# Optimization experiments

Hardware: AMD Instinct MI355X
Metric: run time of the kernel (lower is better)

The kernel has to match this reference:

```python
import jax, jax.numpy as jnp
import numpy as np

N = 80000        # nodes
E = 1280000      # edges
NG = 8           # graphs (segment ids)
F_IN = 3
NC = 20
BN_EPS = 1e-3    # keras BatchNormalization default epsilon


def setup_inputs() -> dict:
    key = jax.random.key(0)
    ks = jax.random.split(key, 16)
    inp = {}
    inp['x'] = jax.random.normal(ks[0], (N, F_IN), dtype=jnp.float32)
    inp['edge_w'] = jax.random.uniform(ks[1], (E,), dtype=jnp.float32)
    inp['src'] = jax.random.randint(ks[2], (E,), 0, N, dtype=jnp.int32)
    inp['dst'] = jax.random.randint(ks[3], (E,), 0, N, dtype=jnp.int32)
    inp['ids'] = jnp.sort(jax.random.randint(ks[4], (N,), 0, NG, dtype=jnp.int32))
    def w(k, fi, fo):
        return jax.random.normal(k, (fi, fo), dtype=jnp.float32) * (1.0 / np.sqrt(fi))
    inp['W1'] = w(ks[5], F_IN, 32); inp['b1'] = jnp.zeros((32,), jnp.float32)
    inp['W2'] = w(ks[6], 32, 32);   inp['b2'] = jnp.zeros((32,), jnp.float32)
    inp['g1'] = jnp.ones((32,), jnp.float32); inp['be1'] = jnp.zeros((32,), jnp.float32)
    inp['m1'] = jax.random.normal(ks[7], (32,), dtype=jnp.float32) * 0.1
    inp['v1'] = jax.random.uniform(ks[8], (32,), dtype=jnp.float32) + 0.5
    inp['W3'] = w(ks[9], 32, 64);   inp['b3'] = jnp.zeros((64,), jnp.float32)
    inp['W4'] = w(ks[10], 64, 64);  inp['b4'] = jnp.zeros((64,), jnp.float32)
    inp['g2'] = jnp.ones((64,), jnp.float32); inp['be2'] = jnp.zeros((64,), jnp.float32)
    inp['m2'] = jax.random.normal(ks[11], (64,), dtype=jnp.float32) * 0.1
    inp['v2'] = jax.random.uniform(ks[12], (64,), dtype=jnp.float32) + 0.5
    inp['W5'] = w(ks[13], 64, NC);  inp['b5'] = jnp.zeros((NC,), jnp.float32)
    return inp


def _gcn(x, W, b, src, dst, ew):
    # Spektral GCNConv: A_norm @ (X W) + b, with A given as edge list (src->dst).
    h = x @ W                                      # [N, Fo] dense transform first (cheaper)
    msg = h[src] * ew[:, None]                     # gather + scale  [E, Fo]
    agg = jax.ops.segment_sum(msg, dst, num_segments=N)  # scatter-add [N, Fo]
    return agg + b


def _bn(x, g, be, m, v):
    # inference-mode BatchNormalization
    return (x - m) * (g * jax.lax.rsqrt(v + BN_EPS)) + be


def _pool(x, ids):
    # per-graph global max pooling, broadcast back to nodes
    mx = jax.ops.segment_max(x, ids, num_segments=NG)   # [NG, F]
    return mx[ids]                                       # [N, F]


def reference(x, edge_w, src, dst, ids,
              W1, b1, W2, b2, g1, be1, m1, v1,
              W3, b3, W4, b4, g2, be2, m2, v2,
              W5, b5):
    h = jax.nn.relu(_gcn(x, W1, b1, src, dst, edge_w))
    h = jax.nn.relu(_gcn(h, W2, b2, src, dst, edge_w))
    h = _bn(h, g1, be1, m1, v1)
    h = _pool(h, ids)
    h = jax.nn.relu(_gcn(h, W3, b3, src, dst, edge_w))
    h = jax.nn.relu(_gcn(h, W4, b4, src, dst, edge_w))
    h = _bn(h, g2, be2, m2, v2)
    h = _pool(h, ids)
    # dropout is identity in inference
    out = jax.nn.softmax(_gcn(h, W5, b5, src, dst, edge_w), axis=-1)
    return out
```

## Files before the change

kernel.cpp:

```cpp
#include <hip/hip_runtime.h>

#define NN 80000
#define NE 1280000
#define NGR 8
#define BN_EPS 1e-3f
#define NBF 625
#define GB 1280
#define CHK 1000

typedef unsigned short ushort;
typedef __attribute__((ext_vector_type(8))) short bf16x8;
typedef __attribute__((ext_vector_type(4))) float f32x4;

__device__ __forceinline__ unsigned enc_f(float f) {
    unsigned b = __float_as_uint(f);
    return (f >= 0.f) ? (b | 0x80000000u) : ~b;
}
__device__ __forceinline__ float dec_f(unsigned u) {
    return (u & 0x80000000u) ? __uint_as_float(u & 0x7FFFFFFFu) : __uint_as_float(~u);
}
__device__ __forceinline__ ushort f2bf(float f) {
    unsigned u = __float_as_uint(f);
    unsigned r = u + 0x7FFFu + ((u >> 16) & 1u);
    return (ushort)(r >> 16);
}
__device__ __forceinline__ void fma8(float* acc, const ushort* p, float w) {
    uint4 q = *(const uint4*)p;
    acc[0] += w * __uint_as_float((q.x & 0xFFFFu) << 16);
    acc[1] += w * __uint_as_float(q.x & 0xFFFF0000u);
    acc[2] += w * __uint_as_float((q.y & 0xFFFFu) << 16);
    acc[3] += w * __uint_as_float(q.y & 0xFFFF0000u);
    acc[4] += w * __uint_as_float((q.z & 0xFFFFu) << 16);
    acc[5] += w * __uint_as_float(q.z & 0xFFFF0000u);
    acc[6] += w * __uint_as_float((q.w & 0xFFFFu) << 16);
    acc[7] += w * __uint_as_float(q.w & 0xFFFF0000u);
}

__global__ __launch_bounds__(256) void k_bhist(const int* __restrict__ dst,
                                               int* __restrict__ hcnt) {
    __shared__ int lh[NBF];
    for (int i = threadIdx.x; i < NBF; i += 256) lh[i] = 0;
    __syncthreads();
    int e0 = blockIdx.x * CHK;
    for (int e = e0 + threadIdx.x; e < e0 + CHK; e += 256)
        atomicAdd(&lh[dst[e] >> 7], 1);
    __syncthreads();
    int* row = hcnt + (size_t)blockIdx.x * NBF;
    for (int i = threadIdx.x; i < NBF; i += 256) row[i] = lh[i];
}

__global__ __launch_bounds__(256) void k_bbase1(int* __restrict__ hcnt,
                                                int* __restrict__ tot) {
    __shared__ int sm[256];
    int bin = blockIdx.x, t = threadIdx.x;
    int v[5];
    int s = 0;
    #pragma unroll
    for (int j = 0; j < 5; ++j) {
        v[j] = hcnt[(size_t)(t * 5 + j) * NBF + bin];
        s += v[j];
    }
    sm[t] = s;
    __syncthreads();
    #pragma unroll
    for (int off = 1; off < 256; off <<= 1) {
        int u = (t >= off) ? sm[t - off] : 0;
        __syncthreads();
        sm[t] += u;
        __syncthreads();
    }
    int run = sm[t] - s;
    if (t == 255) tot[bin] = sm[255];
    #pragma unroll
    for (int j = 0; j < 5; ++j) {
        hcnt[(size_t)(t * 5 + j) * NBF + bin] = run;
        run += v[j];
    }
}

__global__ __launch_bounds__(1024) void k_bbase2w(const int* __restrict__ tot,
                                                  int* __restrict__ bo,
                                                  const float* __restrict__ W2,
                                                  const float* __restrict__ W4,
                                                  ushort* __restrict__ W2t,
                                                  ushort* __restrict__ W4t) {
    __shared__ int sm[1024];
    int t = threadIdx.x;
    int v = (t < NBF) ? tot[t] : 0;
    sm[t] = v;
    __syncthreads();
    #pragma unroll
    for (int off = 1; off < 1024; off <<= 1) {
        int u = (t >= off) ? sm[t - off] : 0;
        __syncthreads();
        sm[t] += u;
        __syncthreads();
    }
    if (t < NBF) bo[t] = sm[t] - v;
    if (t == 0) bo[NBF] = NE;
    {
        int f = t >> 5, k = t & 31;
        W2t[t] = f2bf(W2[k * 32 + f]);
    }
    #pragma unroll
    for (int j = 0; j < 4; ++j) {
        int i = t + j * 1024;
        int f = i >> 6, k = i & 63;
        W4t[i] = f2bf(W4[k * 64 + f]);
    }
}

__global__ __launch_bounds__(256) void k_bfill(const int* __restrict__ src,
                                               const int* __restrict__ dst,
                                               const float* __restrict__ ew,
                                               const int* __restrict__ ids,
                                               const int* __restrict__ hcnt,
                                               const int* __restrict__ bo,
                                               int2* __restrict__ cB) {
    __shared__ int lcur[NBF];
    const int* row = hcnt + (size_t)blockIdx.x * NBF;
    for (int i = threadIdx.x; i < NBF; i += 256) lcur[i] = row[i] + bo[i];
    __syncthreads();
    int e0 = blockIdx.x * CHK;
    for (int e = e0 + threadIdx.x; e < e0 + CHK; e += 256) {
        int d = dst[e];
        int s = src[e];
        int pos = atomicAdd(&lcur[d >> 7], 1);
        cB[pos] = make_int2(s | (ids[s] << 17) | ((d & 127) << 20),
                            __float_as_int(ew[e]));
    }
}

__global__ __launch_bounds__(512) void k_insort(const int* __restrict__ bo,
                                                const int2* __restrict__ cB,
                                                const float* __restrict__ x,
                                                int* __restrict__ rp,
                                                int2* __restrict__ cE,
                                                float* __restrict__ S,
                                                float* __restrict__ AX) {
    __shared__ int lc[128];
    __shared__ int loff[128];
    __shared__ int sm[512];
    int bin = blockIdx.x, t = threadIdx.x;
    int s0 = bo[bin], s1 = bo[bin + 1];
    if (t < 128) lc[t] = 0;
    __syncthreads();
    for (int i = s0 + t; i < s1; i += 512)
        atomicAdd(&lc[(cB[i].x >> 20) & 127], 1);
    __syncthreads();
    int v = (t < 128) ? lc[t] : 0;
    sm[t] = v;
    __syncthreads();
    #pragma unroll
    for (int off = 1; off < 128; off <<= 1) {
        int u = (t >= off && t < 128) ? sm[t - off] : 0;
        __syncthreads();
        if (t < 128) sm[t] += u;
        __syncthreads();
    }
    if (t < 128) {
        loff[t] = sm[t] - v;
        rp[bin * 128 + t] = s0 + loff[t];
        lc[t] = 0;
    }
    if (bin == NBF - 1 && t == 0) rp[NN] = NE;
    __syncthreads();
    for (int i = s0 + t; i < s1; i += 512) {
        int2 a = cB[i];
        int dlow = (a.x >> 20) & 127;
        int pos = s0 + loff[dlow] + atomicAdd(&lc[dlow], 1);
        cE[pos] = make_int2((a.x & 0x1FFFF) | (((a.x >> 17) & 7) << 24), a.y);
    }
    __syncthreads();
    int n = t >> 2, q = t & 3;
    int ne0 = s0 + loff[n];
    int ne1 = ne0 + lc[n];
    float sv[8] = {0, 0, 0, 0, 0, 0, 0, 0};
    float ax0 = 0.f, ax1 = 0.f, ax2 = 0.f;
    for (int i = ne0 + q; i < ne1; i += 4) {
        int2 a = cE[i];
        float w = __int_as_float(a.y);
        int s = a.x & 0xFFFFFF;
        int gg = a.x >> 24;
        #pragma unroll
        for (int g = 0; g < 8; ++g) sv[g] += (gg == g) ? w : 0.f;
        const float* xp = x + s * 3;
        ax0 += w * xp[0]; ax1 += w * xp[1]; ax2 += w * xp[2];
    }
    #pragma unroll
    for (int g = 0; g < 8; ++g) {
        sv[g] += __shfl_xor(sv[g], 1);
        sv[g] += __shfl_xor(sv[g], 2);
    }
    ax0 += __shfl_xor(ax0, 1); ax0 += __shfl_xor(ax0, 2);
    ax1 += __shfl_xor(ax1, 1); ax1 += __shfl_xor(ax1, 2);
    ax2 += __shfl_xor(ax2, 1); ax2 += __shfl_xor(ax2, 2);
    if (q == 0) {
        int node = bin * 128 + n;
        float4* Sp = (float4*)(S + (size_t)node * 8);
        Sp[0] = make_float4(sv[0], sv[1], sv[2], sv[3]);
        Sp[1] = make_float4(sv[4], sv[5], sv[6], sv[7]);
        *(float4*)(AX + (size_t)node * 4) = make_float4(ax0, ax1, ax2, 0.f);
    }
}

__global__ __launch_bounds__(256) void k_l12m(const float* __restrict__ AX,
                                              const float* __restrict__ W1,
                                              const float* __restrict__ b1,
                                              const ushort* __restrict__ W2t,
                                              ushort* __restrict__ T) {
    __shared__ ushort h1s[64 * 40];
    int t = threadIdx.x;
    int nb = blockIdx.x * 64;
    {
        int f = t & 31, rr = t >> 5;
        float w0 = W1[f], w1 = W1[32 + f], w2 = W1[64 + f], bb = b1[f];
        #pragma unroll
        for (int i = 0; i < 8; ++i) {
            int n = rr + i * 8;
            float4 ax = *(const float4*)(AX + (nb + n) * 4);
            float acc = bb + ax.x * w0 + ax.y * w1 + ax.z * w2;
            h1s[n * 40 + f] = f2bf(fmaxf(acc, 0.f));
        }
    }
    __syncthreads();
    int lane = t & 63, wave = t >> 6;
    int quad = lane >> 4, col = lane & 15;
    int mtile = wave;
    bf16x8 a = *(const bf16x8*)(h1s + (mtile * 16 + col) * 40 + quad * 8);
    #pragma unroll
    for (int ntile = 0; ntile < 2; ++ntile) {
        bf16x8 b = *(const bf16x8*)(W2t + (ntile * 16 + col) * 32 + quad * 8);
        f32x4 acc = {0.f, 0.f, 0.f, 0.f};
        acc = __builtin_amdgcn_mfma_f32_16x16x32_bf16(a, b, acc, 0, 0, 0);
        #pragma unroll
        for (int r = 0; r < 4; ++r) {
            int node = nb + mtile * 16 + quad * 4 + r;
            T[node * 32 + ntile * 16 + col] = f2bf(acc[r]);
        }
    }
}

__global__ __launch_bounds__(256) void k_l34m(const float* __restrict__ S,
                                              const unsigned* __restrict__ mxe,
                                              const float* __restrict__ W3,
                                              const float* __restrict__ b3,
                                              const ushort* __restrict__ W4t,
                                              ushort* __restrict__ T) {
    __shared__ float smxs[256];
    __shared__ float HW3s[512];
    __shared__ ushort h3s[64 * 72];
    int t = threadIdx.x;
    int nb = blockIdx.x * 64;
    smxs[t] = mxe[t] ? dec_f(mxe[t]) : 0.f;
    __syncthreads();
    {
        #pragma unroll
        for (int j = 0; j < 2; ++j) {
            int i = t + j * 256;
            int g = i >> 6, f = i & 63;
            float acc = 0.f;
            #pragma unroll
            for (int k = 0; k < 32; ++k) acc += smxs[g * 32 + k] * W3[k * 64 + f];
            HW3s[i] = acc;
        }
    }
    __syncthreads();
    {
        int f = t & 63, rr = t >> 6;
        float hwc[8];
        #pragma unroll
        for (int g = 0; g < 8; ++g) hwc[g] = HW3s[g * 64 + f];
        float bb = b3[f];
        #pragma unroll
        for (int i = 0; i < 16; ++i) {
            int n = rr + i * 4;
            const float4* sp = (const float4*)(S + (size_t)(nb + n) * 8);
            float4 s0 = sp[0], s1 = sp[1];
            float acc = bb + s0.x * hwc[0] + s0.y * hwc[1] + s0.z * hwc[2] +
                        s0.w * hwc[3] + s1.x * hwc[4] + s1.y * hwc[5] +
                        s1.z * hwc[6] + s1.w * hwc[7];
            h3s[n * 72 + f] = f2bf(fmaxf(acc, 0.f));
        }
    }
    __syncthreads();
    int lane = t & 63, wave = t >> 6;
    int quad = lane >> 4, col = lane & 15;
    int mtile = wave;
    bf16x8 a0 = *(const bf16x8*)(h3s + (mtile * 16 + col) * 72 + quad * 8);
    bf16x8 a1 = *(const bf16x8*)(h3s + (mtile * 16 + col) * 72 + 32 + quad * 8);
    #pragma unroll
    for (int ntile = 0; ntile < 4; ++ntile) {
        bf16x8 b0 = *(const bf16x8*)(W4t + (ntile * 16 + col) * 64 + quad * 8);
        bf16x8 b1v = *(const bf16x8*)(W4t + (ntile * 16 + col) * 64 + 32 + quad * 8);
        f32x4 acc = {0.f, 0.f, 0.f, 0.f};
        acc = __builtin_amdgcn_mfma_f32_16x16x32_bf16(a0, b0, acc, 0, 0, 0);
        acc = __builtin_amdgcn_mfma_f32_16x16x32_bf16(a1, b1v, acc, 0, 0, 0);
        #pragma unroll
        for (int r = 0; r < 4; ++r) {
            int node = nb + mtile * 16 + quad * 4 + r;
            T[node * 64 + ntile * 16 + col] = f2bf(acc[r]);
        }
    }
}

template <int LOGF>
__global__ __launch_bounds__(256) void k_gpool(const ushort* __restrict__ th,
                                               const int* __restrict__ rp,
                                               const int2* __restrict__ cE,
                                               const int* __restrict__ ids,
                                               const float* __restrict__ b,
                                               const float* __restrict__ g,
                                               const float* __restrict__ be,
                                               const float* __restrict__ m,
                                               const float* __restrict__ v,
                                               unsigned* __restrict__ mxe) {
    const int F = 1 << LOGF;
    const int CPN = F >> 3;
    const int NPB = 256 / CPN;
    __shared__ unsigned lmx[NGR * F];
    for (int i = threadIdx.x; i < NGR * F; i += 256) lmx[i] = 0u;
    __syncthreads();
    int c = threadIdx.x & (CPN - 1);
    int n = blockIdx.x * NPB + (threadIdx.x >> (LOGF - 3));
    if (n < NN) {
        int e0 = rp[n], e1 = rp[n + 1];
        float a0[8] = {0, 0, 0, 0, 0, 0, 0, 0};
        float a1[8] = {0, 0, 0, 0, 0, 0, 0, 0};
        float a2[8] = {0, 0, 0, 0, 0, 0, 0, 0};
        float a3[8] = {0, 0, 0, 0, 0, 0, 0, 0};
        int i = e0;
        for (; i + 4 <= e1; i += 4) {
            int2 q0 = cE[i], q1 = cE[i + 1], q2 = cE[i + 2], q3 = cE[i + 3];
            fma8(a0, th + (((size_t)(q0.x & 0xFFFFFF)) << LOGF) + (c << 3), __int_as_float(q0.y));
            fma8(a1, th + (((size_t)(q1.x & 0xFFFFFF)) << LOGF) + (c << 3), __int_as_float(q1.y));
            fma8(a2, th + (((size_t)(q2.x & 0xFFFFFF)) << LOGF) + (c << 3), __int_as_float(q2.y));
            fma8(a3, th + (((size_t)(q3.x & 0xFFFFFF)) << LOGF) + (c << 3), __int_as_float(q3.y));
        }
        for (; i < e1; ++i) {
            int2 q0 = cE[i];
            fma8(a0, th + (((size_t)(q0.x & 0xFFFFFF)) << LOGF) + (c << 3), __int_as_float(q0.y));
        }
        int gg = ids[n];
        #pragma unroll
        for (int j = 0; j < 8; ++j) {
            int f = (c << 3) + j;
            float scale = g[f] * rsqrtf(v[f] + BN_EPS);
            float h = fmaxf((a0[j] + a1[j]) + (a2[j] + a3[j]) + b[f], 0.f);
            float val = (h - m[f]) * scale + be[f];
            atomicMax(&lmx[gg * F + f], enc_f(val));
        }
    }
    __syncthreads();
    for (int i = threadIdx.x; i < NGR * F; i += 256) {
        unsigned u = lmx[i];
        if (u) atomicMax(&mxe[i], u);
    }
}

__global__ __launch_bounds__(256) void k_out(const float* __restrict__ S,
                                             const unsigned* __restrict__ mxe,
                                             const float* __restrict__ W5,
                                             const float* __restrict__ b5,
                                             float* __restrict__ out) {
    __shared__ float smxs[512];
    __shared__ float hw[160];
    __shared__ float bb[20];
    int t = threadIdx.x;
    smxs[t] = mxe[t] ? dec_f(mxe[t]) : 0.f;
    smxs[t + 256] = mxe[t + 256] ? dec_f(mxe[t + 256]) : 0.f;
    if (t < 20) bb[t] = b5[t];
    __syncthreads();
    if (t < 160) {
        int g = t / 20, c = t % 20;
        float acc = 0.f;
        #pragma unroll
        for (int k = 0; k < 64; ++k) acc += smxs[g * 64 + k] * W5[k * 20 + c];
        hw[t] = acc;
    }
    __syncthreads();
    int n = blockIdx.x * 256 + t;
    if (n >= NN) return;
    const float4* sp = (const float4*)(S + (size_t)n * 8);
    float4 s0 = sp[0], s1 = sp[1];
    float sv[8] = {s0.x, s0.y, s0.z, s0.w, s1.x, s1.y, s1.z, s1.w};
    float pre[20];
    #pragma unroll
    for (int c = 0; c < 20; ++c) {
        float acc = bb[c];
        #pragma unroll
        for (int g = 0; g < 8; ++g) acc += sv[g] * hw[g * 20 + c];
        pre[c] = acc;
    }
    float mx = pre[0];
    #pragma unroll
    for (int c = 1; c < 20; ++c) mx = fmaxf(mx, pre[c]);
    float sum = 0.f;
    #pragma unroll
    for (int c = 0; c < 20; ++c) { pre[c] = __expf(pre[c] - mx); sum += pre[c]; }
    float inv = 1.f / sum;
    #pragma unroll
    for (int c = 0; c < 20; ++c) out[n * 20 + c] = pre[c] * inv;
}

extern "C" void kernel_launch(void* const* d_in, const int* in_sizes, int n_in,
                              void* d_out, int out_size, void* d_ws, size_t ws_size,
                              hipStream_t stream) {
    const float* x   = (const float*)d_in[0];
    const float* ew  = (const float*)d_in[1];
    const int*   src = (const int*)d_in[2];
    const int*   dst = (const int*)d_in[3];
    const int*   ids = (const int*)d_in[4];
    const float* W1 = (const float*)d_in[5];  const float* b1 = (const float*)d_in[6];
    const float* W2 = (const float*)d_in[7];  const float* b2 = (const float*)d_in[8];
    const float* g1 = (const float*)d_in[9];  const float* be1 = (const float*)d_in[10];
    const float* m1 = (const float*)d_in[11]; const float* v1 = (const float*)d_in[12];
    const float* W3 = (const float*)d_in[13]; const float* b3 = (const float*)d_in[14];
    const float* W4 = (const float*)d_in[15]; const float* b4 = (const float*)d_in[16];
    const float* g2 = (const float*)d_in[17]; const float* be2 = (const float*)d_in[18];
    const float* m2 = (const float*)d_in[19]; const float* v2 = (const float*)d_in[20];
    const float* W5 = (const float*)d_in[21]; const float* b5 = (const float*)d_in[22];
    float* out = (float*)d_out;

    char* p = (char*)d_ws;
    float*  S    = (float*)p;  p += (size_t)NN * 8 * 4;
    ushort* T    = (ushort*)p; p += (size_t)NN * 64 * 2;
    float*  AX   = (float*)p;  p += (size_t)NN * 4 * 4;
    int*    rp   = (int*)p;    p += (size_t)(NN + 16) * 4;
    int*    hcnt = (int*)p;    p += (size_t)GB * NBF * 4;
    int*    tot  = (int*)p;    p += 1024 * 4;
    int*    bo   = (int*)p;    p += 1024 * 4;
    int2*   cB   = (int2*)p;   p += (size_t)NE * 8;
    int2*   cE   = (int2*)p;   p += (size_t)NE * 8;
    unsigned* MXE1 = (unsigned*)p; p += 256 * 4;
    unsigned* MXE2 = (unsigned*)p; p += 512 * 4;
    ushort* W2t  = (ushort*)p; p += 1024 * 2;
    ushort* W4t  = (ushort*)p; p += 4096 * 2;

    const int BS = 256;
    const int gN = (NN + BS - 1) / BS;

    hipMemsetAsync(MXE1, 0, 768 * 4, stream);
    hipLaunchKernelGGL(k_bhist, dim3(GB), dim3(BS), 0, stream, dst, hcnt);
    hipLaunchKernelGGL(k_bbase1, dim3(NBF), dim3(BS), 0, stream, hcnt, tot);
    hipLaunchKernelGGL(k_bbase2w, dim3(1), dim3(1024), 0, stream, tot, bo, W2, W4, W2t, W4t);
    hipLaunchKernelGGL(k_bfill, dim3(GB), dim3(BS), 0, stream, src, dst, ew, ids, hcnt, bo, cB);
    hipLaunchKernelGGL(k_insort, dim3(NBF), dim3(512), 0, stream, bo, cB, x, rp, cE, S, AX);

    hipLaunchKernelGGL(k_l12m, dim3(NN / 64), dim3(BS), 0, stream, AX, W1, b1, W2t, T);
    hipLaunchKernelGGL(k_gpool<5>, dim3(NN / 64), dim3(BS), 0, stream, T, rp, cE, ids, b2, g1, be1, m1, v1, MXE1);

    hipLaunchKernelGGL(k_l34m, dim3(NN / 64), dim3(BS), 0, stream, S, MXE1, W3, b3, W4t, T);
    hipLaunchKernelGGL(k_gpool<6>, dim3(NN / 32), dim3(BS), 0, stream, T, rp, cE, ids, b4, g2, be2, m2, v2, MXE2);

    hipLaunchKernelGGL(k_out, dim3(gN), dim3(BS), 0, stream, S, MXE2, W5, b5, out);
}
```

Measured before the change: 259.0 us.

## Reassociate GCN layers: aggregate before dense transform, fuse into pooling kernels

Layers 2 and 4 now aggregate the previous layer's ReLU output over neighbours first and then apply the weight matrix with MFMA, using (A·H)·W instead of A·(H·W). Neighbour features are recomputed on the fly from the small AX/S arrays, so the intermediate bf16 T buffer and the separate matmul kernels are gone. BN and max-pooling are fused into the same kernel. In exchange, each edge visit recomputes the previous layer's per-node activation, which costs more ALU work per edge but reads much less gathered data.

```diff
diff --git a/kernel.cpp b/kernel.cpp
--- a/kernel.cpp
+++ b/kernel.cpp
@@ -23,17 +23,6 @@
     unsigned u = __float_as_uint(f);
     unsigned r = u + 0x7FFFu + ((u >> 16) & 1u);
     return (ushort)(r >> 16);
-}
-__device__ __forceinline__ void fma8(float* acc, const ushort* p, float w) {
-    uint4 q = *(const uint4*)p;
-    acc[0] += w * __uint_as_float((q.x & 0xFFFFu) << 16);
-    acc[1] += w * __uint_as_float(q.x & 0xFFFF0000u);
-    acc[2] += w * __uint_as_float((q.y & 0xFFFFu) << 16);
-    acc[3] += w * __uint_as_float(q.y & 0xFFFF0000u);
-    acc[4] += w * __uint_as_float((q.z & 0xFFFFu) << 16);
-    acc[5] += w * __uint_as_float(q.z & 0xFFFF0000u);
-    acc[6] += w * __uint_as_float((q.w & 0xFFFFu) << 16);
-    acc[7] += w * __uint_as_float(q.w & 0xFFFF0000u);
 }
 
 __global__ __launch_bounds__(256) void k_bhist(const int* __restrict__ dst,
@@ -204,157 +193,202 @@
     }
 }
 
-__global__ __launch_bounds__(256) void k_l12m(const float* __restrict__ AX,
+__global__ __launch_bounds__(256) void k_gpl2(const float* __restrict__ AX,
                                               const float* __restrict__ W1,
                                               const float* __restrict__ b1,
                                               const ushort* __restrict__ W2t,
-                                              ushort* __restrict__ T) {
-    __shared__ ushort h1s[64 * 40];
+                                              const int* __restrict__ rp,
+                                              const int2* __restrict__ cE,
+                                              const int* __restrict__ ids,
+                                              const float* __restrict__ b2,
+                                              const float* __restrict__ g1,
+                                              const float* __restrict__ be1,
+                                              const float* __restrict__ m1,
+                                              const float* __restrict__ v1,
+                                              unsigned* __restrict__ mxe) {
+    __shared__ unsigned lmx[NGR * 32];
+    __shared__ ushort aggS[64 * 40];
+    __shared__ int gids[64];
     int t = threadIdx.x;
     int nb = blockIdx.x * 64;
-    {
-        int f = t & 31, rr = t >> 5;
-        float w0 = W1[f], w1 = W1[32 + f], w2 = W1[64 + f], bb = b1[f];
-        #pragma unroll
-        for (int i = 0; i < 8; ++i) {
-            int n = rr + i * 8;
-            float4 ax = *(const float4*)(AX + (nb + n) * 4);
-            float acc = bb + ax.x * w0 + ax.y * w1 + ax.z * w2;
-            h1s[n * 40 + f] = f2bf(fmaxf(acc, 0.f));
-        }
-    }
+    lmx[t] = 0u;
+    if (t < 64) gids[t] = ids[nb + t];
+    int c = t & 3;
+    float w1r0[8], w1r1[8], w1r2[8], b1c[8];
+    #pragma unroll
+    for (int j = 0; j < 8; ++j) {
+        int f = c * 8 + j;
+        w1r0[j] = W1[f]; w1r1[j] = W1[32 + f]; w1r2[j] = W1[64 + f];
+        b1c[j] = b1[f];
+    }
+    int nl = t >> 2;
+    int n = nb + nl;
+    int e0 = rp[n], e1 = rp[n + 1];
+    float acc[8] = {0, 0, 0, 0, 0, 0, 0, 0};
+    for (int i = e0; i < e1; ++i) {
+        int2 a = cE[i];
+        float w = __int_as_float(a.y);
+        float axv = AX[(size_t)(a.x & 0xFFFFFF) * 4 + c];
+        float a0 = __shfl(axv, 0, 4);
+        float a1 = __shfl(axv, 1, 4);
+        float a2 = __shfl(axv, 2, 4);
+        #pragma unroll
+        for (int j = 0; j < 8; ++j) {
+            float pre = b1c[j] + a0 * w1r0[j] + a1 * w1r1[j] + a2 * w1r2[j];
+            acc[j] += w * fmaxf(pre, 0.f);
+        }
+    }
+    #pragma unroll
+    for (int j = 0; j < 8; ++j) aggS[nl * 40 + c * 8 + j] = f2bf(acc[j]);
     __syncthreads();
     int lane = t & 63, wave = t >> 6;
     int quad = lane >> 4, col = lane & 15;
-    int mtile = wave;
-    bf16x8 a = *(const bf16x8*)(h1s + (mtile * 16 + col) * 40 + quad * 8);
-    #pragma unroll
-    for (int ntile = 0; ntile < 2; ++ntile) {
-        bf16x8 b = *(const bf16x8*)(W2t + (ntile * 16 + col) * 32 + quad * 8);
-        f32x4 acc = {0.f, 0.f, 0.f, 0.f};
-        acc = __builtin_amdgcn_mfma_f32_16x16x32_bf16(a, b, acc, 0, 0, 0);
+    bf16x8 afr = *(const bf16x8*)(aggS + (wave * 16 + col) * 40 + quad * 8);
+    #pragma unroll
+    for (int nt = 0; nt < 2; ++nt) {
+        bf16x8 bfr = *(const bf16x8*)(W2t + (nt * 16 + col) * 32 + quad * 8);
+        f32x4 d = {0.f, 0.f, 0.f, 0.f};
+        d = __builtin_amdgcn_mfma_f32_16x16x32_bf16(afr, bfr, d, 0, 0, 0);
+        int f = nt * 16 + col;
+        float scale = g1[f] * rsqrtf(v1[f] + BN_EPS);
+        float bb = b2[f], mm = m1[f], bee = be1[f];
         #pragma unroll
         for (int r = 0; r < 4; ++r) {
-            int node = nb + mtile * 16 + quad * 4 + r;
-            T[node * 32 + ntile * 16 + col] = f2bf(acc[r]);
-        }
-    }
-}
-
-__global__ __launch_bounds__(256) void k_l34m(const float* __restrict__ S,
-                                              const unsigned* __restrict__ mxe,
+            int node_l = wave * 16 + quad * 4 + r;
+            float h = fmaxf(d[r] + bb, 0.f);
+            float val = (h - mm) * scale + bee;
+            atomicMax(&lmx[gids[node_l] * 32 + f], enc_f(val));
+        }
+    }
+    __syncthreads();
+    {
+        unsigned u = lmx[t];
+        if (u) atomicMax(&mxe[t], u);
+    }
+}
+
+__global__ __launch_bounds__(256) void k_gpl4(const float* __restrict__ S,
+                                              const unsigned* __restrict__ mxe1,
                                               const float* __restrict__ W3,
                                               const float* __restrict__ b3,
                                               const ushort* __restrict__ W4t,
-                                              ushort* __restrict__ T) {
+                                              const int* __restrict__ rp,
+                                              const int2* __restrict__ cE,
+                                              const int* __restrict__ ids,
+                                              const float* __restrict__ b4,
+                                              const float* __restrict__ g2,
+                                              const float* __restrict__ be2,
+                                              const float* __restrict__ m2,
+                                              const float* __restrict__ v2,
+                                              unsigned* __restrict__ mxe2) {
     __shared__ float smxs[256];
     __shared__ float HW3s[512];
-    __shared__ ushort h3s[64 * 72];
+    __shared__ unsigned lmx[NGR * 64];
+    __shared__ ushort aggS[32 * 72];
+    __shared__ int gids[32];
     int t = threadIdx.x;
-    int nb = blockIdx.x * 64;
-    smxs[t] = mxe[t] ? dec_f(mxe[t]) : 0.f;
-    __syncthreads();
-    {
-        #pragma unroll
-        for (int j = 0; j < 2; ++j) {
-            int i = t + j * 256;
-            int g = i >> 6, f = i & 63;
-            float acc = 0.f;
+    int nb = blockIdx.x * 32;
+    smxs[t] = mxe1[t] ? dec_f(mxe1[t]) : 0.f;
+    lmx[t] = 0u; lmx[t + 256] = 0u;
+    if (t < 32) gids[t] = ids[nb + t];
+    __syncthreads();
+    #pragma unroll
+    for (int jj = 0; jj < 2; ++jj) {
+        int i = t + jj * 256;
+        int g = i >> 6, f = i & 63;
+        float a = 0.f;
+        #pragma unroll
+        for (int k = 0; k < 32; ++k) a += smxs[g * 32 + k] * W3[k * 64 + f];
+        HW3s[i] = a;
+    }
+    __syncthreads();
+    int c = t & 7;
+    float hw[8][8], b3c[8];
+    #pragma unroll
+    for (int j = 0; j < 8; ++j) {
+        int f = c * 8 + j;
+        b3c[j] = b3[f];
+        #pragma unroll
+        for (int k = 0; k < 8; ++k) hw[k][j] = HW3s[k * 64 + f];
+    }
+    int nl = t >> 3;
+    int n = nb + nl;
+    int e0 = rp[n], e1 = rp[n + 1];
+    float acc[8] = {0, 0, 0, 0, 0, 0, 0, 0};
+    float acc2[8] = {0, 0, 0, 0, 0, 0, 0, 0};
+    int i = e0;
+    for (; i + 2 <= e1; i += 2) {
+        int2 a0 = cE[i], a1 = cE[i + 1];
+        float sv0 = S[(size_t)(a0.x & 0xFFFFFF) * 8 + c];
+        float sv1 = S[(size_t)(a1.x & 0xFFFFFF) * 8 + c];
+        float w0 = __int_as_float(a0.y), w1 = __int_as_float(a1.y);
+        float s0k[8], s1k[8];
+        #pragma unroll
+        for (int k = 0; k < 8; ++k) {
+            s0k[k] = __shfl(sv0, k, 8);
+            s1k[k] = __shfl(sv1, k, 8);
+        }
+        #pragma unroll
+        for (int j = 0; j < 8; ++j) {
+            float p0 = b3c[j], p1 = b3c[j];
             #pragma unroll
-            for (int k = 0; k < 32; ++k) acc += smxs[g * 32 + k] * W3[k * 64 + f];
-            HW3s[i] = acc;
-        }
-    }
-    __syncthreads();
-    {
-        int f = t & 63, rr = t >> 6;
-        float hwc[8];
-        #pragma unroll
-        for (int g = 0; g < 8; ++g) hwc[g] = HW3s[g * 64 + f];
-        float bb = b3[f];
-        #pragma unroll
-        for (int i = 0; i < 16; ++i) {
-            int n = rr + i * 4;
-            const float4* sp = (const float4*)(S + (size_t)(nb + n) * 8);
-            float4 s0 = sp[0], s1 = sp[1];
-            float acc = bb + s0.x * hwc[0] + s0.y * hwc[1] + s0.z * hwc[2] +
-                        s0.w * hwc[3] + s1.x * hwc[4] + s1.y * hwc[5] +
-                        s1.z * hwc[6] + s1.w * hwc[7];
-            h3s[n * 72 + f] = f2bf(fmaxf(acc, 0.f));
-        }
-    }
+            for (int k = 0; k < 8; ++k) {
+                p0 += s0k[k] * hw[k][j];
+                p1 += s1k[k] * hw[k][j];
+            }
+            acc[j] += w0 * fmaxf(p0, 0.f);
+            acc2[j] += w1 * fmaxf(p1, 0.f);
+        }
+    }
+    if (i < e1) {
+        int2 a0 = cE[i];
+        float sv0 = S[(size_t)(a0.x & 0xFFFFFF) * 8 + c];
+        float w0 = __int_as_float(a0.y);
+        float s0k[8];
+        #pragma unroll
+        for (int k = 0; k < 8; ++k) s0k[k] = __shfl(sv0, k, 8);
+        #pragma unroll
+        for (int j = 0; j < 8; ++j) {
+            float p0 = b3c[j];
+            #pragma unroll
+            for (int k = 0; k < 8; ++k) p0 += s0k[k] * hw[k][j];
+            acc[j] += w0 * fmaxf(p0, 0.f);
+        }
+    }
+    #pragma unroll
+    for (int j = 0; j < 8; ++j)
+        aggS[nl * 72 + c * 8 + j] = f2bf(acc[j] + acc2[j]);
     __syncthreads();
     int lane = t & 63, wave = t >> 6;
     int quad = lane >> 4, col = lane & 15;
-    int mtile = wave;
-    bf16x8 a0 = *(const bf16x8*)(h3s + (mtile * 16 + col) * 72 + quad * 8);
-    bf16x8 a1 = *(const bf16x8*)(h3s + (mtile * 16 + col) * 72 + 32 + quad * 8);
-    #pragma unroll
-    for (int ntile = 0; ntile < 4; ++ntile) {
-        bf16x8 b0 = *(const bf16x8*)(W4t + (ntile * 16 + col) * 64 + quad * 8);
-        bf16x8 b1v = *(const bf16x8*)(W4t + (ntile * 16 + col) * 64 + 32 + quad * 8);
-        f32x4 acc = {0.f, 0.f, 0.f, 0.f};
-        acc = __builtin_amdgcn_mfma_f32_16x16x32_bf16(a0, b0, acc, 0, 0, 0);
-        acc = __builtin_amdgcn_mfma_f32_16x16x32_bf16(a1, b1v, acc, 0, 0, 0);
+    int mt = wave >> 1;
+    bf16x8 a0f = *(const bf16x8*)(aggS + (mt * 16 + col) * 72 + quad * 8);
+    bf16x8 a1f = *(const bf16x8*)(aggS + (mt * 16 + col) * 72 + 32 + quad * 8);
+    #pragma unroll
+    for (int q = 0; q < 2; ++q) {
+        int nt = (wave & 1) * 2 + q;
+        bf16x8 b0f = *(const bf16x8*)(W4t + (nt * 16 + col) * 64 + quad * 8);
+        bf16x8 b1f = *(const bf16x8*)(W4t + (nt * 16 + col) * 64 + 32 + quad * 8);
+        f32x4 d = {0.f, 0.f, 0.f, 0.f};
+        d = __builtin_amdgcn_mfma_f32_16x16x32_bf16(a0f, b0f, d, 0, 0, 0);
+        d = __builtin_amdgcn_mfma_f32_16x16x32_bf16(a1f, b1f, d, 0, 0, 0);
+        int f = nt * 16 + col;
+        float scale = g2[f] * rsqrtf(v2[f] + BN_EPS);
+        float bb = b4[f], mm = m2[f], bee = be2[f];
         #pragma unroll
         for (int r = 0; r < 4; ++r) {
-            int node = nb + mtile * 16 + quad * 4 + r;
-            T[node * 64 + ntile * 16 + col] = f2bf(acc[r]);
-        }
-    }
-}
-
-template <int LOGF>
-__global__ __launch_bounds__(256) void k_gpool(const ushort* __restrict__ th,
-                                               const int* __restrict__ rp,
-                                               const int2* __restrict__ cE,
-                                               const int* __restrict__ ids,
-                                               const float* __restrict__ b,
-                                               const float* __restrict__ g,
-                                               const float* __restrict__ be,
-                                               const float* __restrict__ m,
-                                               const float* __restrict__ v,
-                                               unsigned* __restrict__ mxe) {
-    const int F = 1 << LOGF;
-    const int CPN = F >> 3;
-    const int NPB = 256 / CPN;
-    __shared__ unsigned lmx[NGR * F];
-    for (int i = threadIdx.x; i < NGR * F; i += 256) lmx[i] = 0u;
-    __syncthreads();
-    int c = threadIdx.x & (CPN - 1);
-    int n = blockIdx.x * NPB + (threadIdx.x >> (LOGF - 3));
-    if (n < NN) {
-        int e0 = rp[n], e1 = rp[n + 1];
-        float a0[8] = {0, 0, 0, 0, 0, 0, 0, 0};
-        float a1[8] = {0, 0, 0, 0, 0, 0, 0, 0};
-        float a2[8] = {0, 0, 0, 0, 0, 0, 0, 0};
-        float a3[8] = {0, 0, 0, 0, 0, 0, 0, 0};
-        int i = e0;
-        for (; i + 4 <= e1; i += 4) {
-            int2 q0 = cE[i], q1 = cE[i + 1], q2 = cE[i + 2], q3 = cE[i + 3];
-            fma8(a0, th + (((size_t)(q0.x & 0xFFFFFF)) << LOGF) + (c << 3), __int_as_float(q0.y));
-            fma8(a1, th + (((size_t)(q1.x & 0xFFFFFF)) << LOGF) + (c << 3), __int_as_float(q1.y));
-            fma8(a2, th + (((size_t)(q2.x & 0xFFFFFF)) << LOGF) + (c << 3), __int_as_float(q2.y));
-            fma8(a3, th + (((size_t)(q3.x & 0xFFFFFF)) << LOGF) + (c << 3), __int_as_float(q3.y));
-        }
-        for (; i < e1; ++i) {
-            int2 q0 = cE[i];
-            fma8(a0, th + (((size_t)(q0.x & 0xFFFFFF)) << LOGF) + (c << 3), __int_as_float(q0.y));
-        }
-        int gg = ids[n];
-        #pragma unroll
-        for (int j = 0; j < 8; ++j) {
-            int f = (c << 3) + j;
-            float scale = g[f] * rsqrtf(v[f] + BN_EPS);
-            float h = fmaxf((a0[j] + a1[j]) + (a2[j] + a3[j]) + b[f], 0.f);
-            float val = (h - m[f]) * scale + be[f];
-            atomicMax(&lmx[gg * F + f], enc_f(val));
-        }
-    }
-    __syncthreads();
-    for (int i = threadIdx.x; i < NGR * F; i += 256) {
-        unsigned u = lmx[i];
-        if (u) atomicMax(&mxe[i], u);
+            int node_l = mt * 16 + quad * 4 + r;
+            float h = fmaxf(d[r] + bb, 0.f);
+            float val = (h - mm) * scale + bee;
+            atomicMax(&lmx[gids[node_l] * 64 + f], enc_f(val));
+        }
+    }
+    __syncthreads();
+    {
+        unsigned u = lmx[t];
+        if (u) atomicMax(&mxe2[t], u);
+        u = lmx[t + 256];
+        if (u) atomicMax(&mxe2[t + 256], u);
     }
 }
 
@@ -424,7 +458,6 @@
 
     char* p = (char*)d_ws;
     float*  S    = (float*)p;  p += (size_t)NN * 8 * 4;
-    ushort* T    = (ushort*)p; p += (size_t)NN * 64 * 2;
     float*  AX   = (float*)p;  p += (size_t)NN * 4 * 4;
     int*    rp   = (int*)p;    p += (size_t)(NN + 16) * 4;
     int*    hcnt = (int*)p;    p += (size_t)GB * NBF * 4;
@@ -447,11 +480,11 @@
     hipLaunchKernelGGL(k_bfill, dim3(GB), dim3(BS), 0, stream, src, dst, ew, ids, hcnt, bo, cB);
     hipLaunchKernelGGL(k_insort, dim3(NBF), dim3(512), 0, stream, bo, cB, x, rp, cE, S, AX);
 
-    hipLaunchKernelGGL(k_l12m, dim3(NN / 64), dim3(BS), 0, stream, AX, W1, b1, W2t, T);
-    hipLaunchKernelGGL(k_gpool<5>, dim3(NN / 64), dim3(BS), 0, stream, T, rp, cE, ids, b2, g1, be1, m1, v1, MXE1);
-
-    hipLaunchKernelGGL(k_l34m, dim3(NN / 64), dim3(BS), 0, stream, S, MXE1, W3, b3, W4t, T);
-    hipLaunchKernelGGL(k_gpool<6>, dim3(NN / 32), dim3(BS), 0, stream, T, rp, cE, ids, b4, g2, be2, m2, v2, MXE2);
+    hipLaunchKernelGGL(k_gpl2, dim3(NN / 64), dim3(BS), 0, stream, AX, W1, b1, W2t,
+                       rp, cE, ids, b2, g1, be1, m1, v1, MXE1);
+
+    hipLaunchKernelGGL(k_gpl4, dim3(NN / 32), dim3(BS), 0, stream, S, MXE1, W3, b3, W4t,
+                       rp, cE, ids, b4, g2, be2, m2, v2, MXE2);
 
     hipLaunchKernelGGL(k_out, dim3(gN), dim3(BS), 0, stream, S, MXE2, W5, b5, out);
 }
```

Result: slower. 291.6 us (+12.6%).

## Fuse layer-1/2 transform into edge aggregation, aggregating before W2 matmul

Applied to the files above, without the earlier changes.

Replaces the separate layer-2 transform kernel and gather/pool kernel with one kernel. Each edge gathers the 3-feature AX row and recomputes relu(AX·W1+b1) on the fly. The result is aggregated per node, then multiplied by W2 via MFMA with bias, relu, BN and per-graph max fused in. This avoids writing and re-reading the 32-feature intermediate and shrinks gather traffic per edge, at the cost of extra per-edge arithmetic and a 4-threads-per-node layout.

```diff
diff --git a/kernel.cpp b/kernel.cpp
--- a/kernel.cpp
+++ b/kernel.cpp
@@ -204,40 +204,77 @@
     }
 }
 
-__global__ __launch_bounds__(256) void k_l12m(const float* __restrict__ AX,
+__global__ __launch_bounds__(256) void k_gpl2(const float* __restrict__ AX,
                                               const float* __restrict__ W1,
                                               const float* __restrict__ b1,
                                               const ushort* __restrict__ W2t,
-                                              ushort* __restrict__ T) {
-    __shared__ ushort h1s[64 * 40];
+                                              const int* __restrict__ rp,
+                                              const int2* __restrict__ cE,
+                                              const int* __restrict__ ids,
+                                              const float* __restrict__ b2,
+                                              const float* __restrict__ g1,
+                                              const float* __restrict__ be1,
+                                              const float* __restrict__ m1,
+                                              const float* __restrict__ v1,
+                                              unsigned* __restrict__ mxe) {
+    __shared__ unsigned lmx[NGR * 32];
+    __shared__ ushort aggS[64 * 40];
+    __shared__ int gids[64];
     int t = threadIdx.x;
     int nb = blockIdx.x * 64;
-    {
-        int f = t & 31, rr = t >> 5;
-        float w0 = W1[f], w1 = W1[32 + f], w2 = W1[64 + f], bb = b1[f];
-        #pragma unroll
-        for (int i = 0; i < 8; ++i) {
-            int n = rr + i * 8;
-            float4 ax = *(const float4*)(AX + (nb + n) * 4);
-            float acc = bb + ax.x * w0 + ax.y * w1 + ax.z * w2;
-            h1s[n * 40 + f] = f2bf(fmaxf(acc, 0.f));
-        }
-    }
+    lmx[t] = 0u;
+    if (t < 64) gids[t] = ids[nb + t];
+    int c = t & 3;
+    float w1r0[8], w1r1[8], w1r2[8], b1c[8];
+    #pragma unroll
+    for (int j = 0; j < 8; ++j) {
+        int f = c * 8 + j;
+        w1r0[j] = W1[f]; w1r1[j] = W1[32 + f]; w1r2[j] = W1[64 + f];
+        b1c[j] = b1[f];
+    }
+    int nl = t >> 2;
+    int n = nb + nl;
+    int e0 = rp[n], e1 = rp[n + 1];
+    float acc[8] = {0, 0, 0, 0, 0, 0, 0, 0};
+    for (int i = e0; i < e1; ++i) {
+        int2 a = cE[i];
+        float w = __int_as_float(a.y);
+        float axv = AX[(size_t)(a.x & 0xFFFFFF) * 4 + c];
+        float a0 = __shfl(axv, 0, 4);
+        float a1 = __shfl(axv, 1, 4);
+        float a2 = __shfl(axv, 2, 4);
+        #pragma unroll
+        for (int j = 0; j < 8; ++j) {
+            float pre = b1c[j] + a0 * w1r0[j] + a1 * w1r1[j] + a2 * w1r2[j];
+            acc[j] += w * fmaxf(pre, 0.f);
+        }
+    }
+    #pragma unroll
+    for (int j = 0; j < 8; ++j) aggS[nl * 40 + c * 8 + j] = f2bf(acc[j]);
     __syncthreads();
     int lane = t & 63, wave = t >> 6;
     int quad = lane >> 4, col = lane & 15;
-    int mtile = wave;
-    bf16x8 a = *(const bf16x8*)(h1s + (mtile * 16 + col) * 40 + quad * 8);
-    #pragma unroll
-    for (int ntile = 0; ntile < 2; ++ntile) {
-        bf16x8 b = *(const bf16x8*)(W2t + (ntile * 16 + col) * 32 + quad * 8);
-        f32x4 acc = {0.f, 0.f, 0.f, 0.f};
-        acc = __builtin_amdgcn_mfma_f32_16x16x32_bf16(a, b, acc, 0, 0, 0);
+    bf16x8 afr = *(const bf16x8*)(aggS + (wave * 16 + col) * 40 + quad * 8);
+    #pragma unroll
+    for (int nt = 0; nt < 2; ++nt) {
+        bf16x8 bfr = *(const bf16x8*)(W2t + (nt * 16 + col) * 32 + quad * 8);
+        f32x4 d = {0.f, 0.f, 0.f, 0.f};
+        d = __builtin_amdgcn_mfma_f32_16x16x32_bf16(afr, bfr, d, 0, 0, 0);
+        int f = nt * 16 + col;
+        float scale = g1[f] * rsqrtf(v1[f] + BN_EPS);
+        float bb = b2[f], mm = m1[f], bee = be1[f];
         #pragma unroll
         for (int r = 0; r < 4; ++r) {
-            int node = nb + mtile * 16 + quad * 4 + r;
-            T[node * 32 + ntile * 16 + col] = f2bf(acc[r]);
-        }
+            int node_l = wave * 16 + quad * 4 + r;
+            float h = fmaxf(d[r] + bb, 0.f);
+            float val = (h - mm) * scale + bee;
+            atomicMax(&lmx[gids[node_l] * 32 + f], enc_f(val));
+        }
+    }
+    __syncthreads();
+    {
+        unsigned u = lmx[t];
+        if (u) atomicMax(&mxe[t], u);
     }
 }
 
@@ -447,8 +484,8 @@
     hipLaunchKernelGGL(k_bfill, dim3(GB), dim3(BS), 0, stream, src, dst, ew, ids, hcnt, bo, cB);
     hipLaunchKernelGGL(k_insort, dim3(NBF), dim3(512), 0, stream, bo, cB, x, rp, cE, S, AX);
 
-    hipLaunchKernelGGL(k_l12m, dim3(NN / 64), dim3(BS), 0, stream, AX, W1, b1, W2t, T);
-    hipLaunchKernelGGL(k_gpool<5>, dim3(NN / 64), dim3(BS), 0, stream, T, rp, cE, ids, b2, g1, be1, m1, v1, MXE1);
+    hipLaunchKernelGGL(k_gpl2, dim3(NN / 64), dim3(BS), 0, stream, AX, W1, b1, W2t,
+                       rp, cE, ids, b2, g1, be1, m1, v1, MXE1);
 
     hipLaunchKernelGGL(k_l34m, dim3(NN / 64), dim3(BS), 0, stream, S, MXE1, W3, b3, W4t, T);
     hipLaunchKernelGGL(k_gpool<6>, dim3(NN / 32), dim3(BS), 0, stream, T, rp, cE, ids, b4, g2, be2, m2, v2, MXE2);
```

After: 248.3 us. 4.1% less time.
